# Kernel tuning notes

Measured on AMD Instinct MI355X. Metric: run time of the kernel, lower is better.

The kernel has to match this reference:

```python
import jax, jax.numpy as jnp
import numpy as np

P = 1024
H, W = 160, 160
TANFOVX = 0.5
TANFOVY = 0.5
SCALE_MODIFIER = 1.0


def _quat_to_rot(q):
    # q: [P,4] normalized quaternions (r, x, y, z)
    r, x, y, z = q[:, 0], q[:, 1], q[:, 2], q[:, 3]
    row0 = jnp.stack([1 - 2 * (y * y + z * z), 2 * (x * y - r * z), 2 * (x * z + r * y)], -1)
    row1 = jnp.stack([2 * (x * y + r * z), 1 - 2 * (x * x + z * z), 2 * (y * z - r * x)], -1)
    row2 = jnp.stack([2 * (x * z - r * y), 2 * (y * z + r * x), 1 - 2 * (x * x + y * y)], -1)
    return jnp.stack([row0, row1, row2], -2)  # [P,3,3]


def _rasterize(means3D, colors_precomp, opacities, scales, rotations, bg, viewmatrix, projmatrix):
    fx = W / (2.0 * TANFOVX)
    fy = H / (2.0 * TANFOVY)

    hom = jnp.concatenate([means3D, jnp.ones((means3D.shape[0], 1), means3D.dtype)], -1)  # [P,4]
    t = hom @ viewmatrix.T  # view space [P,4]
    tz = t[:, 2]
    depth_ok = tz > 0.2  # near-plane cull as in CUDA kernel

    p_hom = hom @ projmatrix.T
    p_w = 1.0 / (p_hom[:, 3] + 1e-7)
    p_proj = p_hom[:, :3] * p_w[:, None]
    # ndc2pix
    px = ((p_proj[:, 0] + 1.0) * W - 1.0) * 0.5
    py = ((p_proj[:, 1] + 1.0) * H - 1.0) * 0.5

    # 3D covariance: Sigma = R S S^T R^T
    s = scales * SCALE_MODIFIER
    R = _quat_to_rot(rotations)
    M = R * s[:, None, :]  # R @ diag(s)
    cov3D = M @ jnp.swapaxes(M, 1, 2)  # [P,3,3]

    # EWA projection to 2D covariance
    limx = 1.3 * TANFOVX
    limy = 1.3 * TANFOVY
    txz = jnp.clip(t[:, 0] / tz, -limx, limx) * tz
    tyz = jnp.clip(t[:, 1] / tz, -limy, limy) * tz
    zero = jnp.zeros_like(tz)
    J = jnp.stack([
        jnp.stack([fx / tz, zero, -fx * txz / (tz * tz)], -1),
        jnp.stack([zero, fy / tz, -fy * tyz / (tz * tz)], -1),
    ], -2)  # [P,2,3]
    Wm = viewmatrix[:3, :3]
    T = jnp.einsum('pij,jk->pik', J, Wm)  # [P,2,3]
    cov2 = jnp.einsum('pij,pjk,plk->pil', T, cov3D, T)  # [P,2,2]
    a = cov2[:, 0, 0] + 0.3  # low-pass filter on diagonal
    c = cov2[:, 1, 1] + 0.3
    b = cov2[:, 0, 1]
    det = a * c - b * b
    det_ok = det > 0
    inv_det = jnp.where(det_ok, 1.0 / jnp.where(det_ok, det, 1.0), 0.0)
    conic_a = c * inv_det
    conic_b = -b * inv_det
    conic_c = a * inv_det

    mid = 0.5 * (a + c)
    lam1 = mid + jnp.sqrt(jnp.maximum(0.1, mid * mid - det))
    radius = jnp.ceil(3.0 * jnp.sqrt(lam1))

    valid = depth_ok & det_ok
    radii = jnp.where(valid, radius, 0.0).astype(jnp.int32)

    # per-pixel Gaussian evaluation
    ys, xs = jnp.meshgrid(jnp.arange(H, dtype=means3D.dtype), jnp.arange(W, dtype=means3D.dtype), indexing='ij')
    dx = px[:, None, None] - xs[None]  # [P,H,W]
    dy = py[:, None, None] - ys[None]
    power = (-0.5 * (conic_a[:, None, None] * dx * dx + conic_c[:, None, None] * dy * dy)
             - conic_b[:, None, None] * dx * dy)
    op = opacities[:, 0][:, None, None]
    alpha = jnp.minimum(0.99, op * jnp.exp(power))
    alpha = jnp.where((power > 0.0) | (alpha < 1.0 / 255.0) | (~valid)[:, None, None], 0.0, alpha)

    # front-to-back alpha compositing in depth order
    depth_key = jnp.where(valid, tz, jnp.inf)
    order = jnp.argsort(depth_key)
    alpha_s = alpha[order]            # [P,H,W]
    colors_s = colors_precomp[order]  # [P,3]
    Tcum = jnp.cumprod(1.0 - alpha_s, axis=0)
    Texcl = jnp.concatenate([jnp.ones((1, H, W), alpha_s.dtype), Tcum[:-1]], 0)
    w = alpha_s * Texcl
    color = jnp.einsum('phw,pc->chw', w, colors_s) + Tcum[-1][None] * bg[:, None, None]
    return color, radii


def setup_inputs() -> dict:
    key = jax.random.key(0)
    ks = jax.random.split(key, 6)
    u = jax.random.uniform(ks[0], (P, 3), dtype=jnp.float32)
    means3D = jnp.stack([u[:, 0] * 4 - 2, u[:, 1] * 4 - 2, u[:, 2] * 6 + 2], -1)  # inside frustum
    means2D = jnp.zeros((P, 3), jnp.float32)  # gradient-holder only, unused in fwd
    colors_precomp = jax.random.uniform(ks[1], (P, 3), dtype=jnp.float32)
    opacities = jax.random.uniform(ks[2], (P, 1), dtype=jnp.float32) * 0.9 + 0.05
    scales = jax.random.uniform(ks[3], (P, 3), dtype=jnp.float32) * 0.15 + 0.05
    q = jax.random.normal(ks[4], (P, 4), dtype=jnp.float32)
    rotations = q / jnp.linalg.norm(q, axis=-1, keepdims=True)
    bg = jnp.zeros((3,), jnp.float32)
    viewmatrix = jnp.eye(4, dtype=jnp.float32)
    znear, zfar = 0.01, 100.0
    persp = jnp.array([[1.0 / TANFOVX, 0, 0, 0],
                       [0, 1.0 / TANFOVY, 0, 0],
                       [0, 0, zfar / (zfar - znear), -zfar * znear / (zfar - znear)],
                       [0, 0, 1.0, 0]], dtype=jnp.float32)
    projmatrix = persp @ viewmatrix
    campos = jnp.zeros((3,), jnp.float32)
    return dict(means3D=means3D, means2D=means2D, colors_precomp=colors_precomp,
                opacities=opacities, scales=scales, rotations=rotations,
                bg=bg, viewmatrix=viewmatrix, projmatrix=projmatrix, campos=campos)


def reference(means3D, means2D, colors_precomp, opacities, scales, rotations, bg, viewmatrix, projmatrix, campos):
    color, radii = _rasterize(means3D, colors_precomp, opacities, scales, rotations, bg, viewmatrix, projmatrix)
    return color, radii
```

## Files before the change

### kernel.cpp

```cpp
#include <hip/hip_runtime.h>
#include <math.h>

#define PCNT 1024
#define HH 160
#define WW 160
#define NPIX (HH * WW)
#define TILE 8
#define TX (WW / TILE)
#define TY (HH / TILE)
#define NTILES (TX * TY)
#define NBLK 256

__global__ __launch_bounds__(512) void k_all(
    const float* __restrict__ means, const float* __restrict__ cols,
    const float* __restrict__ ops, const float* __restrict__ scales,
    const float* __restrict__ rots, const float* __restrict__ vm,
    const float* __restrict__ pm, const float* __restrict__ bg,
    float* __restrict__ out)
{
    __shared__ float4 sp[PCNT * 3];
    __shared__ float4 cl[PCNT];
    __shared__ unsigned int kbits[PCNT];
    __shared__ unsigned long long sl[2][PCNT];
    __shared__ unsigned short ranked[2][PCNT];
    __shared__ float4 part[2][4][64];
    __shared__ unsigned long long masks[2][16];
    __shared__ int offs[2][16];
    __shared__ int sn[2];

    int tid = threadIdx.x;
    int bid = blockIdx.x;
    int wave = tid >> 6, lane = tid & 63;
    int group = wave >> 2;
    int gwave = wave & 3;
    int gtid = tid & 255;

    const float HL2E = 0.72134752044448170f;
    const float L2E  = 1.4426950408889634f;
    const float LN2  = 0.69314718055994531f;

    for (int i = tid; i < PCNT; i += 512) {
        float mx = means[3 * i], my = means[3 * i + 1], mz = means[3 * i + 2];

        float t0 = vm[0] * mx + vm[1] * my + vm[2] * mz + vm[3];
        float t1 = vm[4] * mx + vm[5] * my + vm[6] * mz + vm[7];
        float t2 = vm[8] * mx + vm[9] * my + vm[10] * mz + vm[11];
        bool depth_ok = t2 > 0.2f;

        float ph0 = pm[0] * mx + pm[1] * my + pm[2] * mz + pm[3];
        float ph1 = pm[4] * mx + pm[5] * my + pm[6] * mz + pm[7];
        float ph3 = pm[12] * mx + pm[13] * my + pm[14] * mz + pm[15];
        float pw = 1.0f / (ph3 + 1e-7f);
        float px = ((ph0 * pw + 1.0f) * (float)WW - 1.0f) * 0.5f;
        float py = ((ph1 * pw + 1.0f) * (float)HH - 1.0f) * 0.5f;

        float4 q = *(const float4*)(rots + 4 * i);
        float qr = q.x, qx = q.y, qy = q.z, qz = q.w;
        float R00 = 1.f - 2.f * (qy * qy + qz * qz), R01 = 2.f * (qx * qy - qr * qz), R02 = 2.f * (qx * qz + qr * qy);
        float R10 = 2.f * (qx * qy + qr * qz), R11 = 1.f - 2.f * (qx * qx + qz * qz), R12 = 2.f * (qy * qz - qr * qx);
        float R20 = 2.f * (qx * qz - qr * qy), R21 = 2.f * (qy * qz + qr * qx), R22 = 1.f - 2.f * (qx * qx + qy * qy);

        float s0 = scales[3 * i], s1 = scales[3 * i + 1], s2 = scales[3 * i + 2];
        float M00 = R00 * s0, M01 = R01 * s1, M02 = R02 * s2;
        float M10 = R10 * s0, M11 = R11 * s1, M12 = R12 * s2;
        float M20 = R20 * s0, M21 = R21 * s1, M22 = R22 * s2;
        float c00 = M00 * M00 + M01 * M01 + M02 * M02;
        float c01 = M00 * M10 + M01 * M11 + M02 * M12;
        float c02 = M00 * M20 + M01 * M21 + M02 * M22;
        float c11 = M10 * M10 + M11 * M11 + M12 * M12;
        float c12 = M10 * M20 + M11 * M21 + M12 * M22;
        float c22 = M20 * M20 + M21 * M21 + M22 * M22;

        const float fx = 160.0f, fy = 160.0f;
        const float limx = 0.65f, limy = 0.65f;
        float txz = fminf(limx, fmaxf(-limx, t0 / t2)) * t2;
        float tyz = fminf(limy, fmaxf(-limy, t1 / t2)) * t2;
        float rz = 1.0f / t2;
        float J00 = fx * rz, J02 = -fx * txz * rz * rz;
        float J11 = fy * rz, J12 = -fy * tyz * rz * rz;

        float T00 = J00 * vm[0] + J02 * vm[8];
        float T01 = J00 * vm[1] + J02 * vm[9];
        float T02 = J00 * vm[2] + J02 * vm[10];
        float T10 = J11 * vm[4] + J12 * vm[8];
        float T11 = J11 * vm[5] + J12 * vm[9];
        float T12 = J11 * vm[6] + J12 * vm[10];

        float u00 = T00 * c00 + T01 * c01 + T02 * c02;
        float u01 = T00 * c01 + T01 * c11 + T02 * c12;
        float u02 = T00 * c02 + T01 * c12 + T02 * c22;
        float u10 = T10 * c00 + T11 * c01 + T12 * c02;
        float u11 = T10 * c01 + T11 * c11 + T12 * c12;
        float u12 = T10 * c02 + T11 * c12 + T12 * c22;
        float a  = u00 * T00 + u01 * T01 + u02 * T02 + 0.3f;
        float bb = u00 * T10 + u01 * T11 + u02 * T12;
        float cc = u10 * T10 + u11 * T11 + u12 * T12 + 0.3f;

        float det = a * cc - bb * bb;
        bool det_ok = det > 0.0f;
        float inv_det = det_ok ? 1.0f / det : 0.0f;
        float conA = cc * inv_det, conB = -bb * inv_det, conC = a * inv_det;
        float mid = 0.5f * (a + cc);
        float lam1 = mid + sqrtf(fmaxf(0.1f, mid * mid - det));
        float radius = ceilf(3.0f * sqrtf(lam1));
        bool valid = depth_ok && det_ok;

        if (bid == 0)
            out[3 * NPIX + i] = valid ? (float)(int)radius : 0.0f;

        if (valid) {
            float op = ops[i];
            float l2; asm("v_log_f32 %0, %1" : "=v"(l2) : "v"(255.0f * op));
            float tau = fmaxf(fmaf(l2, LN2, 0.02f), 0.0f);
            float hx = sqrtf(2.0f * tau * a);
            float hy = sqrtf(2.0f * tau * cc);
            sp[i * 3 + 0] = make_float4(px, py, conA * HL2E, conB * L2E);
            sp[i * 3 + 1] = make_float4(conC * HL2E, op, cols[3 * i], cols[3 * i + 1]);
            sp[i * 3 + 2] = make_float4(cols[3 * i + 2], 0.f, 0.f, 0.f);
            cl[i] = make_float4(px, py, hx, hy);
            kbits[i] = __float_as_uint(t2);
        } else {
            sp[i * 3 + 0] = make_float4(0.f, 0.f, 0.f, 0.f);
            sp[i * 3 + 1] = make_float4(0.f, 0.f, 0.f, 0.f);
            sp[i * 3 + 2] = make_float4(0.f, 0.f, 0.f, 0.f);
            cl[i] = make_float4(0.f, 0.f, -1e9f, -1e9f);
            kbits[i] = 0x7f800000u;
        }
    }
    __syncthreads();

    int tile = bid + group * NBLK;
    bool tvalid = tile < NTILES;
    int tx = tile % TX, ty = tile / TX;
    float x0 = (float)(tx * TILE), y0 = (float)(ty * TILE);

    #pragma unroll
    for (int k = 0; k < 4; ++k) {
        int c = gwave * 4 + k;
        float4 cv = cl[c * 64 + lane];
        bool ov = tvalid &
                  (cv.x + cv.z >= x0 - 1.0f) & (cv.x - cv.z <= x0 + (float)TILE) &
                  (cv.y + cv.w >= y0 - 1.0f) & (cv.y - cv.w <= y0 + (float)TILE);
        unsigned long long m = __ballot(ov);
        if (lane == 0) masks[group][c] = m;
    }
    __syncthreads();
    if (gtid == 0) {
        int acc = 0;
        #pragma unroll
        for (int c = 0; c < 16; ++c) { offs[group][c] = acc; acc += __popcll(masks[group][c]); }
        sn[group] = acc;
    }
    __syncthreads();
    #pragma unroll
    for (int k = 0; k < 4; ++k) {
        int c = gwave * 4 + k;
        unsigned long long m = masks[group][c];
        if ((m >> lane) & 1ull) {
            int g = c * 64 + lane;
            int pos = offs[group][c] + __popcll(m & ((1ull << lane) - 1ull));
            sl[group][pos] = ((unsigned long long)kbits[g] << 32) | (unsigned int)g;
        }
    }
    __syncthreads();
    int n = sn[group];

    for (int t = gtid; t < n; t += 256) {
        unsigned long long key = sl[group][t];
        int cnt = 0, k = 0;
        for (; k + 4 <= n; k += 4) {
            cnt += (sl[group][k]     < key) ? 1 : 0;
            cnt += (sl[group][k + 1] < key) ? 1 : 0;
            cnt += (sl[group][k + 2] < key) ? 1 : 0;
            cnt += (sl[group][k + 3] < key) ? 1 : 0;
        }
        for (; k < n; ++k) cnt += (sl[group][k] < key) ? 1 : 0;
        ranked[group][cnt] = (unsigned short)(key & 1023u);
    }
    __syncthreads();

    float fxp = x0 + (float)(lane & 7);
    float fyp = y0 + (float)(lane >> 3);

    float T = 1.0f, C0 = 0.f, C1 = 0.f, C2 = 0.f;
    int per = (n + 3) >> 2;
    int lo = gwave * per, hi = min(n, lo + per);
    for (int i = lo; i < hi; ++i) {
        int id = ranked[group][i];
        float4 v0 = sp[id * 3 + 0];
        float4 v1 = sp[id * 3 + 1];
        float4 v2 = sp[id * 3 + 2];
        float dx = v0.x - fxp, dy = v0.y - fyp;
        float p = -(v0.z * dx * dx + v1.x * dy * dy) - v0.w * dx * dy;
        float e; asm("v_exp_f32 %0, %1" : "=v"(e) : "v"(p));
        float al = fminf(0.99f, v1.y * e);
        if (p > 0.0f || al < (1.0f / 255.0f)) al = 0.0f;
        float w = al * T;
        C0 = fmaf(w, v1.z, C0);
        C1 = fmaf(w, v1.w, C1);
        C2 = fmaf(w, v2.x, C2);
        T *= (1.0f - al);
    }

    part[group][gwave][lane] = make_float4(C0, C1, C2, T);
    __syncthreads();

    if (tvalid && gtid < 64) {
        float Tt = 1.0f, c0 = 0.f, c1 = 0.f, c2 = 0.f;
        #pragma unroll
        for (int s = 0; s < 4; ++s) {
            float4 v = part[group][s][gtid];
            c0 = fmaf(Tt, v.x, c0);
            c1 = fmaf(Tt, v.y, c1);
            c2 = fmaf(Tt, v.z, c2);
            Tt *= v.w;
        }
        int pix = (ty * TILE + (gtid >> 3)) * WW + tx * TILE + (gtid & 7);
        out[pix]            = c0 + Tt * bg[0];
        out[NPIX + pix]     = c1 + Tt * bg[1];
        out[2 * NPIX + pix] = c2 + Tt * bg[2];
    }
}

extern "C" void kernel_launch(void* const* d_in, const int* in_sizes, int n_in,
                              void* d_out, int out_size, void* d_ws, size_t ws_size,
                              hipStream_t stream) {
    const float* means  = (const float*)d_in[0];
    const float* cols   = (const float*)d_in[2];
    const float* ops    = (const float*)d_in[3];
    const float* scales = (const float*)d_in[4];
    const float* rots   = (const float*)d_in[5];
    const float* bg     = (const float*)d_in[6];
    const float* vm     = (const float*)d_in[7];
    const float* pm     = (const float*)d_in[8];

    float* out = (float*)d_out;

    k_all<<<NBLK, 512, 0, stream>>>(means, cols, ops, scales, rots, vm, pm, bg, out);
}
```

Before: 15.83 us.

## Give idle group's waves to single-tile blocks and vectorize rank-sort compares

Blocks whose second tile would be out of range now put all eight waves on one tile, splitting the ordered Gaussian list eight ways instead of four so no waves sit idle. The splat parameter array is split into separate SoA arrays so the blend loop reads two float4s and one float instead of three float4s. The rank-sort inner loop reads the key list as 16-byte pairs after padding it with max keys, and the tile-overlap test is tightened to the exact pixel range. The cost is extra index arithmetic and non-unrolled loops with runtime trip counts.

Measured after the change: 14.93 us. 5.7% less time.

```diff
diff --git a/kernel.cpp b/kernel.cpp
--- a/kernel.cpp
+++ b/kernel.cpp
@@ -18,12 +18,14 @@
     const float* __restrict__ pm, const float* __restrict__ bg,
     float* __restrict__ out)
 {
-    __shared__ float4 sp[PCNT * 3];
+    __shared__ float4 spA[PCNT];
+    __shared__ float4 spB[PCNT];
+    __shared__ float  spC[PCNT];
     __shared__ float4 cl[PCNT];
     __shared__ unsigned int kbits[PCNT];
-    __shared__ unsigned long long sl[2][PCNT];
+    __shared__ __align__(16) unsigned long long sl[2][PCNT];
     __shared__ unsigned short ranked[2][PCNT];
-    __shared__ float4 part[2][4][64];
+    __shared__ float4 part[8][64];
     __shared__ unsigned long long masks[2][16];
     __shared__ int offs[2][16];
     __shared__ int sn[2];
@@ -31,9 +33,13 @@
     int tid = threadIdx.x;
     int bid = blockIdx.x;
     int wave = tid >> 6, lane = tid & 63;
-    int group = wave >> 2;
-    int gwave = wave & 3;
-    int gtid = tid & 255;
+
+    bool two = (bid + NBLK) < NTILES;
+    int gsz   = two ? 4 : 8;
+    int group = two ? (wave >> 2) : 0;
+    int gwave = two ? (wave & 3) : wave;
+    int gtid  = tid - group * (gsz << 6);
+    int cpw   = 16 / gsz;
 
     const float HL2E = 0.72134752044448170f;
     const float L2E  = 1.4426950408889634f;
@@ -114,15 +120,15 @@
             float tau = fmaxf(fmaf(l2, LN2, 0.02f), 0.0f);
             float hx = sqrtf(2.0f * tau * a);
             float hy = sqrtf(2.0f * tau * cc);
-            sp[i * 3 + 0] = make_float4(px, py, conA * HL2E, conB * L2E);
-            sp[i * 3 + 1] = make_float4(conC * HL2E, op, cols[3 * i], cols[3 * i + 1]);
-            sp[i * 3 + 2] = make_float4(cols[3 * i + 2], 0.f, 0.f, 0.f);
+            spA[i] = make_float4(px, py, conA * HL2E, conB * L2E);
+            spB[i] = make_float4(conC * HL2E, op, cols[3 * i], cols[3 * i + 1]);
+            spC[i] = cols[3 * i + 2];
             cl[i] = make_float4(px, py, hx, hy);
             kbits[i] = __float_as_uint(t2);
         } else {
-            sp[i * 3 + 0] = make_float4(0.f, 0.f, 0.f, 0.f);
-            sp[i * 3 + 1] = make_float4(0.f, 0.f, 0.f, 0.f);
-            sp[i * 3 + 2] = make_float4(0.f, 0.f, 0.f, 0.f);
+            spA[i] = make_float4(0.f, 0.f, 0.f, 0.f);
+            spB[i] = make_float4(0.f, 0.f, 0.f, 0.f);
+            spC[i] = 0.f;
             cl[i] = make_float4(0.f, 0.f, -1e9f, -1e9f);
             kbits[i] = 0x7f800000u;
         }
@@ -130,17 +136,14 @@
     __syncthreads();
 
     int tile = bid + group * NBLK;
-    bool tvalid = tile < NTILES;
     int tx = tile % TX, ty = tile / TX;
     float x0 = (float)(tx * TILE), y0 = (float)(ty * TILE);
 
-    #pragma unroll
-    for (int k = 0; k < 4; ++k) {
-        int c = gwave * 4 + k;
+    for (int k = 0; k < cpw; ++k) {
+        int c = gwave * cpw + k;
         float4 cv = cl[c * 64 + lane];
-        bool ov = tvalid &
-                  (cv.x + cv.z >= x0 - 1.0f) & (cv.x - cv.z <= x0 + (float)TILE) &
-                  (cv.y + cv.w >= y0 - 1.0f) & (cv.y - cv.w <= y0 + (float)TILE);
+        bool ov = (cv.x + cv.z >= x0) & (cv.x - cv.z <= x0 + (float)(TILE - 1)) &
+                  (cv.y + cv.w >= y0) & (cv.y - cv.w <= y0 + (float)(TILE - 1));
         unsigned long long m = __ballot(ov);
         if (lane == 0) masks[group][c] = m;
     }
@@ -152,9 +155,8 @@
         sn[group] = acc;
     }
     __syncthreads();
-    #pragma unroll
-    for (int k = 0; k < 4; ++k) {
-        int c = gwave * 4 + k;
+    for (int k = 0; k < cpw; ++k) {
+        int c = gwave * cpw + k;
         unsigned long long m = masks[group][c];
         if ((m >> lane) & 1ull) {
             int g = c * 64 + lane;
@@ -164,17 +166,22 @@
     }
     __syncthreads();
     int n = sn[group];
-
-    for (int t = gtid; t < n; t += 256) {
+    for (int t = n + gtid; t < ((n + 3) & ~3) && t < PCNT; t += 64 * gsz)
+        sl[group][t] = ~0ull;
+    __syncthreads();
+
+    for (int t = gtid; t < n; t += 64 * gsz) {
         unsigned long long key = sl[group][t];
-        int cnt = 0, k = 0;
-        for (; k + 4 <= n; k += 4) {
-            cnt += (sl[group][k]     < key) ? 1 : 0;
-            cnt += (sl[group][k + 1] < key) ? 1 : 0;
-            cnt += (sl[group][k + 2] < key) ? 1 : 0;
-            cnt += (sl[group][k + 3] < key) ? 1 : 0;
-        }
-        for (; k < n; ++k) cnt += (sl[group][k] < key) ? 1 : 0;
+        int cnt = 0;
+        const unsigned long long* base = sl[group];
+        for (int k = 0; k < n; k += 4) {
+            ulonglong2 p0 = *(const ulonglong2*)(base + k);
+            ulonglong2 p1 = *(const ulonglong2*)(base + k + 2);
+            cnt += (p0.x < key) ? 1 : 0;
+            cnt += (p0.y < key) ? 1 : 0;
+            cnt += (p1.x < key) ? 1 : 0;
+            cnt += (p1.y < key) ? 1 : 0;
+        }
         ranked[group][cnt] = (unsigned short)(key & 1023u);
     }
     __syncthreads();
@@ -183,13 +190,13 @@
     float fyp = y0 + (float)(lane >> 3);
 
     float T = 1.0f, C0 = 0.f, C1 = 0.f, C2 = 0.f;
-    int per = (n + 3) >> 2;
+    int per = (n + gsz - 1) / gsz;
     int lo = gwave * per, hi = min(n, lo + per);
     for (int i = lo; i < hi; ++i) {
         int id = ranked[group][i];
-        float4 v0 = sp[id * 3 + 0];
-        float4 v1 = sp[id * 3 + 1];
-        float4 v2 = sp[id * 3 + 2];
+        float4 v0 = spA[id];
+        float4 v1 = spB[id];
+        float cb2 = spC[id];
         float dx = v0.x - fxp, dy = v0.y - fyp;
         float p = -(v0.z * dx * dx + v1.x * dy * dy) - v0.w * dx * dy;
         float e; asm("v_exp_f32 %0, %1" : "=v"(e) : "v"(p));
@@ -198,18 +205,18 @@
         float w = al * T;
         C0 = fmaf(w, v1.z, C0);
         C1 = fmaf(w, v1.w, C1);
-        C2 = fmaf(w, v2.x, C2);
+        C2 = fmaf(w, cb2, C2);
         T *= (1.0f - al);
     }
 
-    part[group][gwave][lane] = make_float4(C0, C1, C2, T);
-    __syncthreads();
-
-    if (tvalid && gtid < 64) {
+    part[wave][lane] = make_float4(C0, C1, C2, T);
+    __syncthreads();
+
+    if (gtid < 64) {
         float Tt = 1.0f, c0 = 0.f, c1 = 0.f, c2 = 0.f;
-        #pragma unroll
-        for (int s = 0; s < 4; ++s) {
-            float4 v = part[group][s][gtid];
+        int sbase = group * gsz;
+        for (int s = 0; s < gsz; ++s) {
+            float4 v = part[sbase + s][gtid];
             c0 = fmaf(Tt, v.x, c0);
             c1 = fmaf(Tt, v.y, c1);
             c2 = fmaf(Tt, v.z, c2);
```
